# Kernel optimization log

Hardware: AMD Instinct MI355X
Metric: run time of the kernel (lower is better)

## Reference

```python
import jax, jax.numpy as jnp
import numpy as np

R = 32          # grid_res
G = 32          # num_groups
SQRT2 = 1.4142135623730951


def leaky(x):
    return jax.nn.leaky_relu(x)  # slope 0.01, same as torch default


def group_norm(x, gamma, beta, eps=1e-5):
    # x: [B, C, D, H, W]
    B, C = x.shape[0], x.shape[1]
    xr = x.reshape(B, G, -1)
    mu = xr.mean(-1, keepdims=True)
    var = xr.var(-1, keepdims=True)
    xn = ((xr - mu) * jax.lax.rsqrt(var + eps)).reshape(x.shape)
    s = (1, C, 1, 1, 1)
    return xn * gamma.reshape(s) + beta.reshape(s)


def conv3d(x, w, b):
    # x: [B,C,D,H,W], w: [O,I,k,k,k]
    y = jax.lax.conv_general_dilated(x, w, (1, 1, 1), 'SAME',
                                     dimension_numbers=('NCDHW', 'OIDHW', 'NCDHW'))
    return y + b.reshape(1, -1, 1, 1, 1)


_OFFS = jnp.array([[i, j, k] for i in (0, 1) for j in (0, 1) for k in (0, 1)], jnp.int32)  # [8,3]


def _corners(points):
    # points in [-1,1]^3 -> trilinear corner indices + weights
    coords = jnp.clip((points + 1.0) * 0.5 * (R - 1), 0.0, R - 1.0)   # [B,N,3]
    lo = jnp.clip(jnp.floor(coords), 0.0, R - 2.0)
    frac = coords - lo                                                # [B,N,3]
    lo = lo.astype(jnp.int32)
    idx3 = lo[:, :, None, :] + _OFFS[None, None]                      # [B,N,8,3]
    w = jnp.prod(jnp.where(_OFFS[None, None].astype(bool),
                           frac[:, :, None, :], 1.0 - frac[:, :, None, :]), axis=-1)  # [B,N,8]
    flat = (idx3[..., 0] * R + idx3[..., 1]) * R + idx3[..., 2]       # [B,N,8]
    return flat, w


def voxelize_points3d(points, features):
    # trilinear scatter + weight-normalized average -> [B,R,R,R,C]
    flat, w = _corners(points)
    B, _, C = features.shape

    def per_b(fl, wt, ft):
        vals = (wt[..., None] * ft[:, None, :]).reshape(-1, C)        # [N*8,C]
        g = jnp.zeros((R ** 3, C), ft.dtype).at[fl.reshape(-1)].add(vals)
        cnt = jnp.zeros((R ** 3, 1), ft.dtype).at[fl.reshape(-1)].add(wt.reshape(-1, 1))
        return g / jnp.maximum(cnt, 1e-8)

    grid = jax.vmap(per_b)(flat, w, features)                         # [B,R^3,C]
    return grid.reshape(B, R, R, R, C)


def devoxelize_points3d(points, grid):
    # trilinear gather from [B,R,R,R,C] -> [B,N,C]
    flat, w = _corners(points)
    gf = grid.reshape(grid.shape[0], R ** 3, grid.shape[-1])
    return jax.vmap(lambda fl, wt, g: jnp.einsum('nkc,nk->nc', g[fl], wt))(flat, w, gf)


def setup_inputs() -> dict:
    key = jax.random.key(0)
    ks = jax.random.split(key, 16)
    B, N, Cin, C = 8, 32768, 64, 64
    points = jax.random.uniform(ks[0], (B, N, 3), jnp.float32) * 2.0 - 1.0
    features = jax.random.normal(ks[1], (B, N, Cin), jnp.float32)
    s = 0.05
    return {
        'points': points, 'features': features,
        'w_pi': jax.random.normal(ks[2], (Cin, C), jnp.float32) * s,
        'b_pi': jnp.zeros((C,), jnp.float32),
        'w_p1': jax.random.normal(ks[3], (C, C), jnp.float32) * s,
        'b_p1': jnp.zeros((C,), jnp.float32),
        'w_p2': jax.random.normal(ks[4], (C, C), jnp.float32) * s,
        'b_p2': jnp.zeros((C,), jnp.float32),
        'g1': jnp.ones((Cin,), jnp.float32), 'be1': jnp.zeros((Cin,), jnp.float32),
        'w_c1': jax.random.normal(ks[5], (C, Cin, 3, 3, 3), jnp.float32) * s,
        'b_c1': jnp.zeros((C,), jnp.float32),
        'g2': jnp.ones((C,), jnp.float32), 'be2': jnp.zeros((C,), jnp.float32),
        'w_c2': jax.random.normal(ks[6], (C, C, 3, 3, 3), jnp.float32) * s,
        'b_c2': jnp.zeros((C,), jnp.float32),
    }


def reference(points, features, w_pi, b_pi, w_p1, b_p1, w_p2, b_p2,
              g1, be1, w_c1, b_c1, g2, be2, w_c2, b_c2):
    # voxel branch
    input_grid = jnp.moveaxis(voxelize_points3d(points, features), -1, 1)  # [B,C,R,R,R]
    g = conv3d(leaky(group_norm(input_grid, g1, be1)), w_c1, b_c1)
    g = conv3d(leaky(group_norm(g, g2, be2)), w_c2, b_c2)
    out_grid = jnp.moveaxis(g + input_grid, 1, -1) / SQRT2              # skip: input_dim == dim
    dev = devoxelize_points3d(points, out_grid)                         # [B,N,C]
    # point branch
    f0 = features @ w_pi + b_pi
    h = leaky(f0) @ w_p1 + b_p1
    h = leaky(h) @ w_p2 + b_p2
    pts = (h + f0) / SQRT2
    return (pts + dev) / SQRT2
```

## Files before the change

kernel.cpp:

```cpp
#include <hip/hip_runtime.h>


#define RSQRT2 0.70710678118654752440f

typedef float f32x4 __attribute__((ext_vector_type(4)));
typedef __bf16 bf16x8 __attribute__((ext_vector_type(8)));

static __device__ __forceinline__ unsigned short f2bf(float x) {
    union { float f; unsigned u; } v; v.f = x;
    unsigned r = v.u + 0x7FFFu + ((v.u >> 16) & 1u);
    return (unsigned short)(r >> 16);
}
static __device__ __forceinline__ float bf2f(unsigned short b) {
    union { unsigned u; float f; } v; v.u = ((unsigned)b) << 16; return v.f;
}
static __device__ __forceinline__ float leaky(float x) { return x >= 0.f ? x : 0.01f * x; }

static __device__ __forceinline__ void gload_lds16(const void* g, void* l) {
    __builtin_amdgcn_global_load_lds(
        (const __attribute__((address_space(1))) unsigned int*)g,
        (__attribute__((address_space(3))) unsigned int*)l, 16, 0, 0);
}

static __device__ __forceinline__ void corner_setup(float px, float py, float pz,
        int& lx, int& ly, int& lz, float& fx, float& fy, float& fz) {
    float cx = fminf(fmaxf((px + 1.f) * 15.5f, 0.f), 31.f);
    float cy = fminf(fmaxf((py + 1.f) * 15.5f, 0.f), 31.f);
    float cz = fminf(fmaxf((pz + 1.f) * 15.5f, 0.f), 31.f);
    lx = (int)cx; if (lx > 30) lx = 30; fx = cx - (float)lx;
    ly = (int)cy; if (ly > 30) ly = 30; fy = cy - (float)ly;
    lz = (int)cz; if (lz > 30) lz = 30; fz = cz - (float)lz;
}

__global__ __launch_bounds__(256) void wt_transform(const float* __restrict__ w,
                                                    unsigned short* __restrict__ hi,
                                                    unsigned short* __restrict__ lo) {
    int idx = blockIdx.x * 256 + threadIdx.x;
    int ko = idx >> 12;
    int co = (idx >> 6) & 63;
    int ci = idx & 63;
    float v = w[(co * 64 + ci) * 27 + ko];
    unsigned short h = f2bf(v);
    hi[idx] = h;
    lo[idx] = f2bf(v - bf2f(h));
}

__global__ __launch_bounds__(256) void mlp_wt(const float* __restrict__ w0,
                                              const float* __restrict__ w1,
                                              const float* __restrict__ w2,
                                              unsigned short* __restrict__ hi,
                                              unsigned short* __restrict__ lo) {
    int idx = blockIdx.x * 256 + threadIdx.x;
    int L = idx >> 12, rem = idx & 4095;
    int co = rem >> 6, ci = rem & 63;
    const float* s = (L == 0) ? w0 : (L == 1) ? w1 : w2;
    float v = s[ci * 64 + co];
    unsigned short h = f2bf(v);
    hi[idx] = h;
    lo[idx] = f2bf(v - bf2f(h));
}

__global__ __launch_bounds__(256) void bin_count(const float* __restrict__ pts,
                                                 int* __restrict__ cnt) {
    int p = blockIdx.x * 256 + threadIdx.x;
    int lx, ly, lz; float fx, fy, fz;
    corner_setup(pts[p * 3], pts[p * 3 + 1], pts[p * 3 + 2], lx, ly, lz, fx, fy, fz);
    int b = p >> 15;
    int rx = lx >> 2, ry = ly >> 2, rz = lz >> 2;
    int mx = (lx & 3) == 3, my = (ly & 3) == 3, mz = (lz & 3) == 3;
#pragma unroll
    for (int d = 0; d < 8; ++d) {
        int dx = d >> 2, dy = (d >> 1) & 1, dz = d & 1;
        if (dx <= mx && dy <= my && dz <= mz) {
            int bin = (b << 9) | ((rx + dx) << 6) | ((ry + dy) << 3) | (rz + dz);
            atomicAdd(&cnt[bin], 1);
        }
    }
}

__global__ __launch_bounds__(256) void bin_scan(const int* __restrict__ cnt,
                                                int* __restrict__ start,
                                                int* __restrict__ cursor) {
    __shared__ int part[256];
    int t = threadIdx.x;
    int local[16];
    int s = 0;
#pragma unroll
    for (int i = 0; i < 16; ++i) { local[i] = s; s += cnt[t * 16 + i]; }
    part[t] = s;
    __syncthreads();
    for (int off = 1; off < 256; off <<= 1) {
        int v = (t >= off) ? part[t - off] : 0;
        __syncthreads();
        part[t] += v;
        __syncthreads();
    }
    int base = (t == 0) ? 0 : part[t - 1];
#pragma unroll
    for (int i = 0; i < 16; ++i) {
        int v = base + local[i];
        start[t * 16 + i] = v;
        cursor[t * 16 + i] = v;
    }
    if (t == 255) start[4096] = part[255];
}

__global__ __launch_bounds__(256) void bin_fill(const float* __restrict__ pts,
                                                int* __restrict__ cursor,
                                                unsigned int* __restrict__ idxb,
                                                float4* __restrict__ f3) {
    int p = blockIdx.x * 256 + threadIdx.x;
    int lx, ly, lz; float fx, fy, fz;
    corner_setup(pts[p * 3], pts[p * 3 + 1], pts[p * 3 + 2], lx, ly, lz, fx, fy, fz);
    int b = p >> 15;
    int rx = lx >> 2, ry = ly >> 2, rz = lz >> 2;
    int mx = (lx & 3) == 3, my = (ly & 3) == 3, mz = (lz & 3) == 3;
    float4 fr; fr.x = fx; fr.y = fy; fr.z = fz; fr.w = 0.f;
#pragma unroll
    for (int d = 0; d < 8; ++d) {
        int dx = d >> 2, dy = (d >> 1) & 1, dz = d & 1;
        if (dx <= mx && dy <= my && dz <= mz) {
            int bin = (b << 9) | ((rx + dx) << 6) | ((ry + dy) << 3) | (rz + dz);
            int slot = atomicAdd(&cursor[bin], 1);
            unsigned ux = (unsigned)((lx & 3) - 4 * dx + 1);
            unsigned uy = (unsigned)((ly & 3) - 4 * dy + 1);
            unsigned uz = (unsigned)((lz & 3) - 4 * dz + 1);
            idxb[slot] = (unsigned)p | (ux << 18) | (uy << 21) | (uz << 24);
            f3[slot] = fr;
        }
    }
}

__global__ __launch_bounds__(256) void vox_accum(const float* __restrict__ feat,
                                                 const int* __restrict__ start,
                                                 const unsigned int* __restrict__ idxb,
                                                 const float4* __restrict__ f3,
                                                 float* __restrict__ vox,
                                                 float* __restrict__ chsum) {
    __shared__ float slab[4096];
    __shared__ float cws4[4][64];
    __shared__ float cwsum[64];
    __shared__ float rs[256], rq[256];
    int tid = threadIdx.x, lane = tid & 63, wv = tid >> 6;
    int gid = blockIdx.x;
    int b = gid >> 9, r3 = gid & 511;
    int rx = r3 >> 6, ry = (r3 >> 3) & 7, rz = r3 & 7;
    int cx0 = rx << 2, cy0 = ry << 2, cz0 = rz << 2;
    int cx = lane >> 4, cy = (lane >> 2) & 3, cz = lane & 3;

    f32x4 acc[16] = {};
    float cwr = 0.f;

    int s0 = start[gid], s1 = start[gid + 1];
    for (int e = s0 + wv; e < s1; e += 4) {
        unsigned pk = idxb[e];
        float4 fr = f3[e];
        int pid = __builtin_amdgcn_readfirstlane((int)(pk & 0x3FFFFu));
        int qx = (int)((pk >> 18) & 7u) - 1;
        int qy = (int)((pk >> 21) & 7u) - 1;
        int qz = (int)((pk >> 24) & 7u) - 1;
        float wx = (cx == qx) ? (1.f - fr.x) : ((cx == qx + 1) ? fr.x : 0.f);
        float wy = (cy == qy) ? (1.f - fr.y) : ((cy == qy + 1) ? fr.y : 0.f);
        float wz = (cz == qz) ? (1.f - fr.z) : ((cz == qz + 1) ? fr.z : 0.f);
        float w = wx * wy * wz;
        cwr += w;
        const f32x4* fp = (const f32x4*)(feat + ((size_t)pid << 6));
        f32x4 fa[8];
#pragma unroll
        for (int k = 0; k < 8; ++k) fa[k] = fp[k];
#pragma unroll
        for (int k = 0; k < 8; ++k) acc[k] += fa[k] * w;
#pragma unroll
        for (int k = 0; k < 8; ++k) fa[k] = fp[8 + k];
#pragma unroll
        for (int k = 0; k < 8; ++k) acc[8 + k] += fa[k] * w;
    }

    cws4[wv][lane] = cwr;
#pragma unroll
    for (int ph = 0; ph < 4; ++ph) {
        if (wv == ph) {
#pragma unroll
            for (int k = 0; k < 64; ++k) {
                int addr = (lane << 6) + ((k + lane) & 63);
                float v = acc[k >> 2][k & 3];
                if (ph) v += slab[addr];
                slab[addr] = v;
            }
        }
        __syncthreads();
    }
    if (tid < 64)
        cwsum[tid] = cws4[0][tid] + cws4[1][tid] + cws4[2][tid] + cws4[3][tid];
    __syncthreads();

    float s = 0.f, q = 0.f;
    for (int c = wv; c < 64; c += 4) {
        float v = slab[(c << 6) + ((lane + c) & 63)] / fmaxf(cwsum[c], 1e-8f);
        int cxx = cx0 + (c >> 4), cyy = cy0 + ((c >> 2) & 3), czz = cz0 + (c & 3);
        size_t flat = ((size_t)(b << 15)) + (size_t)((cxx << 10) | (cyy << 5) | czz);
        vox[(flat << 6) + lane] = v;
        s += v; q += v * v;
    }
    rs[tid] = s; rq[tid] = q;
    __syncthreads();
    if (tid < 64) {
        s = rs[tid] + rs[tid + 64] + rs[tid + 128] + rs[tid + 192];
        q = rq[tid] + rq[tid + 64] + rq[tid + 128] + rq[tid + 192];
        atomicAdd(&chsum[((b << 6) + tid) * 2], s);
        atomicAdd(&chsum[((b << 6) + tid) * 2 + 1], q);
    }
}

__global__ __launch_bounds__(256) void norm_stats(const float* __restrict__ src,
                                                  float* __restrict__ chsum) {
    __shared__ float rs[256], rq[256];
    int b = blockIdx.y;
    int tid = threadIdx.x;
    int c = tid & 63, rsub = tid >> 6;
    size_t rowb = ((size_t)b << 15) + (size_t)blockIdx.x * 256;
    float s = 0.f, q = 0.f;
    for (int i = 0; i < 64; ++i) {
        size_t idx = ((rowb + rsub + i * 4) << 6) + c;
        float v = src[idx];
        s += v; q += v * v;
    }
    rs[tid] = s; rq[tid] = q;
    __syncthreads();
    if (tid < 64) {
        s = rs[tid] + rs[tid + 64] + rs[tid + 128] + rs[tid + 192];
        q = rq[tid] + rq[tid + 64] + rq[tid + 128] + rq[tid + 192];
        atomicAdd(&chsum[((b << 6) + tid) * 2], s);
        atomicAdd(&chsum[((b << 6) + tid) * 2 + 1], q);
    }
}

__global__ void gn_finalize(const float* __restrict__ chsum, float* __restrict__ musr) {
    int t = threadIdx.x;
    int b = t >> 5, g = t & 31;
    float s = chsum[((b << 6) + 2 * g) * 2] + chsum[((b << 6) + 2 * g + 1) * 2];
    float q = chsum[((b << 6) + 2 * g) * 2 + 1] + chsum[((b << 6) + 2 * g + 1) * 2 + 1];
    float mu = s * (1.f / 65536.f);
    float var = q * (1.f / 65536.f) - mu * mu;
    musr[t * 2] = mu;
    musr[t * 2 + 1] = rsqrtf(var + 1e-5f);
}

__global__ __launch_bounds__(256) void gn_apply(const float* __restrict__ src,
                                                const float* __restrict__ musr,
                                                const float* __restrict__ gamma,
                                                const float* __restrict__ beta,
                                                unsigned short* __restrict__ hi,
                                                unsigned short* __restrict__ lo) {
    int i4 = blockIdx.x * 256 + threadIdx.x;
    int row = i4 >> 4;
    int b = row >> 15;
    int c0 = (i4 & 15) << 2;
    const float4 x = *(const float4*)(src + ((size_t)i4 << 2));
    float xs[4] = {x.x, x.y, x.z, x.w};
    unsigned short hs[4], ls[4];
#pragma unroll
    for (int j = 0; j < 4; ++j) {
        int c = c0 + j;
        int g = c >> 1;
        float mu = musr[((b << 5) + g) * 2];
        float rstd = musr[((b << 5) + g) * 2 + 1];
        float y = (xs[j] - mu) * rstd * gamma[c] + beta[c];
        y = leaky(y);
        hs[j] = f2bf(y);
        ls[j] = f2bf(y - bf2f(hs[j]));
    }
    ushort4 H; H.x = hs[0]; H.y = hs[1]; H.z = hs[2]; H.w = hs[3];
    ushort4 L; L.x = ls[0]; L.y = ls[1]; L.z = ls[2]; L.w = ls[3];
    *(ushort4*)(hi + ((size_t)i4 << 2)) = H;
    *(ushort4*)(lo + ((size_t)i4 << 2)) = L;
}

__global__ __launch_bounds__(256, 2) void conv3d_k(
        const unsigned short* __restrict__ Ah, const unsigned short* __restrict__ Al,
        const unsigned short* __restrict__ Wh, const unsigned short* __restrict__ Wl,
        const float* __restrict__ bias, const float* __restrict__ skip,
        float* __restrict__ out, const char* __restrict__ zp) {
    __shared__ __align__(16) unsigned short sAh[16384], sAl[16384], sWh[4096], sWl[4096];
    int tid = threadIdx.x;
    int lane = tid & 63, wave = tid >> 6;
    int wg = blockIdx.x;
    int sw = (wg & 7) * 128 + (wg >> 3);
    int b = sw >> 7, t = sw & 127;
    int w0 = (t & 3) << 3, h0 = ((t >> 2) & 3) << 3, d0 = (t >> 4) << 2;

    f32x4 acc[4][4] = {};
    const char* AhB = (const char*)Ah;
    const char* AlB = (const char*)Al;
    const char* WhB = (const char*)Wh;
    const char* WlB = (const char*)Wl;

    for (int ko = 0; ko < 27; ++ko) {
        int di = ko / 9, rem = ko - di * 9, dj = rem / 3, dk = rem - dj * 3;
        __syncthreads();
#pragma unroll
        for (int i = 0; i < 8; ++i) {
            int X = (i * 256 + tid) << 4;
            int row = X >> 7;
            int gran = ((X >> 4) & 7) ^ (row & 7);
            int d = row >> 6, h = (row >> 3) & 7, w = row & 7;
            int gd = d0 + d + di - 1, gh = h0 + h + dj - 1, gw = w0 + w + dk - 1;
            bool ok = ((unsigned)gd < 32u) & ((unsigned)gh < 32u) & ((unsigned)gw < 32u);
            size_t goff = ((((size_t)(b << 15)) +
                            (size_t)((gd << 10) + (gh << 5) + gw)) << 7) + (gran << 4);
            const char* gph = ok ? (AhB + goff) : (zp + (gran << 4));
            const char* gpl = ok ? (AlB + goff) : (zp + (gran << 4));
            int ldsoff = (i * 256 + (wave << 6)) << 4;
            gload_lds16(gph, (char*)sAh + ldsoff);
            gload_lds16(gpl, (char*)sAl + ldsoff);
        }
#pragma unroll
        for (int i = 0; i < 2; ++i) {
            int X = (i * 256 + tid) << 4;
            int row = X >> 7;
            int gran = ((X >> 4) & 7) ^ (row & 7);
            size_t goff = ((size_t)((ko << 12) + (row << 6) + (gran << 3))) << 1;
            int ldsoff = (i * 256 + (wave << 6)) << 4;
            gload_lds16(WhB + goff, (char*)sWh + ldsoff);
            gload_lds16(WlB + goff, (char*)sWl + ldsoff);
        }
        __syncthreads();
#pragma unroll
        for (int kh = 0; kh < 2; ++kh) {
            bf16x8 a_h[4], a_l[4], b_h[4], b_l[4];
#pragma unroll
            for (int mf = 0; mf < 4; ++mf) {
                int arow = (wave << 6) + (mf << 4) + (lane & 15);
                int byteoff = (arow << 7) | ((((kh << 2) | (lane >> 4)) ^ (arow & 7)) << 4);
                a_h[mf] = *(const bf16x8*)((const char*)sAh + byteoff);
                a_l[mf] = *(const bf16x8*)((const char*)sAl + byteoff);
            }
#pragma unroll
            for (int nf = 0; nf < 4; ++nf) {
                int brow = (nf << 4) + (lane & 15);
                int byteoff = (brow << 7) | ((((kh << 2) | (lane >> 4)) ^ (brow & 7)) << 4);
                b_h[nf] = *(const bf16x8*)((const char*)sWh + byteoff);
                b_l[nf] = *(const bf16x8*)((const char*)sWl + byteoff);
            }
#pragma unroll
            for (int mf = 0; mf < 4; ++mf)
#pragma unroll
                for (int nf = 0; nf < 4; ++nf) {
                    acc[mf][nf] = __builtin_amdgcn_mfma_f32_16x16x32_bf16(a_h[mf], b_h[nf], acc[mf][nf], 0, 0, 0);
                    acc[mf][nf] = __builtin_amdgcn_mfma_f32_16x16x32_bf16(a_h[mf], b_l[nf], acc[mf][nf], 0, 0, 0);
                    acc[mf][nf] = __builtin_amdgcn_mfma_f32_16x16x32_bf16(a_l[mf], b_h[nf], acc[mf][nf], 0, 0, 0);
                }
        }
    }
#pragma unroll
    for (int mf = 0; mf < 4; ++mf) {
#pragma unroll
        for (int nf = 0; nf < 4; ++nf) {
            int co = (nf << 4) + (lane & 15);
            float bv = bias[co];
#pragma unroll
            for (int r = 0; r < 4; ++r) {
                int vrow = (wave << 6) + (mf << 4) + ((lane >> 4) << 2) + r;
                int d = vrow >> 6, h = (vrow >> 3) & 7, w = vrow & 7;
                size_t flat = ((size_t)(b << 15)) +
                              (size_t)(((d0 + d) << 10) + ((h0 + h) << 5) + (w0 + w));
                size_t oi = (flat << 6) + co;
                float v = acc[mf][nf][r] + bv;
                if (skip) v = (v + skip[oi]) * RSQRT2;
                out[oi] = v;
            }
        }
    }
}

__global__ __launch_bounds__(256, 2) void point_mlp(
        const float* __restrict__ feat,
        const unsigned short* __restrict__ Mh, const unsigned short* __restrict__ Ml,
        const float* __restrict__ b0, const float* __restrict__ b1,
        const float* __restrict__ b2, float* __restrict__ pout) {
    __shared__ __align__(16) unsigned short sAh[16384], sAl[16384], sWh[4096], sWl[4096];
    int tid = threadIdx.x, lane = tid & 63, wave = tid >> 6;
    size_t pbase = (size_t)blockIdx.x << 8;

    const float4* f4 = (const float4*)(feat + (pbase << 6));
#pragma unroll
    for (int j = 0; j < 16; ++j) {
        int fidx = j * 256 + tid;
        float4 v = f4[fidx];
        float vv[4] = {v.x, v.y, v.z, v.w};
        unsigned short hh[4], ll[4];
#pragma unroll
        for (int k = 0; k < 4; ++k) { hh[k] = f2bf(vv[k]); ll[k] = f2bf(vv[k] - bf2f(hh[k])); }
        ushort4 H; H.x = hh[0]; H.y = hh[1]; H.z = hh[2]; H.w = hh[3];
        ushort4 Lo; Lo.x = ll[0]; Lo.y = ll[1]; Lo.z = ll[2]; Lo.w = ll[3];
        int Xb = fidx << 3;
        int row = Xb >> 7;
        int dest = (row << 7) | ((((Xb >> 4) & 7) ^ (row & 7)) << 4) | (Xb & 8);
        *(ushort4*)((char*)sAh + dest) = H;
        *(ushort4*)((char*)sAl + dest) = Lo;
    }

    f32x4 f0[4][4];
#pragma unroll
    for (int L = 0; L < 3; ++L) {
        __syncthreads();
#pragma unroll
        for (int i = 0; i < 2; ++i) {
            int X = (i * 256 + tid) << 4;
            int row = X >> 7;
            int gran = ((X >> 4) & 7) ^ (row & 7);
            size_t goff = ((size_t)((L << 12) + (row << 6) + (gran << 3))) << 1;
            int ldsoff = (i * 256 + (wave << 6)) << 4;
            gload_lds16((const char*)Mh + goff, (char*)sWh + ldsoff);
            gload_lds16((const char*)Ml + goff, (char*)sWl + ldsoff);
        }
        __syncthreads();
        f32x4 acc[4][4] = {};
#pragma unroll
        for (int kh = 0; kh < 2; ++kh) {
            bf16x8 a_h[4], a_l[4], b_h[4], b_l[4];
#pragma unroll
            for (int mf = 0; mf < 4; ++mf) {
                int arow = (wave << 6) + (mf << 4) + (lane & 15);
                int byteoff = (arow << 7) | ((((kh << 2) | (lane >> 4)) ^ (arow & 7)) << 4);
                a_h[mf] = *(const bf16x8*)((const char*)sAh + byteoff);
                a_l[mf] = *(const bf16x8*)((const char*)sAl + byteoff);
            }
#pragma unroll
            for (int nf = 0; nf < 4; ++nf) {
                int brow = (nf << 4) + (lane & 15);
                int byteoff = (brow << 7) | ((((kh << 2) | (lane >> 4)) ^ (brow & 7)) << 4);
                b_h[nf] = *(const bf16x8*)((const char*)sWh + byteoff);
                b_l[nf] = *(const bf16x8*)((const char*)sWl + byteoff);
            }
#pragma unroll
            for (int mf = 0; mf < 4; ++mf)
#pragma unroll
                for (int nf = 0; nf < 4; ++nf) {
                    acc[mf][nf] = __builtin_amdgcn_mfma_f32_16x16x32_bf16(a_h[mf], b_h[nf], acc[mf][nf], 0, 0, 0);
                    acc[mf][nf] = __builtin_amdgcn_mfma_f32_16x16x32_bf16(a_h[mf], b_l[nf], acc[mf][nf], 0, 0, 0);
                    acc[mf][nf] = __builtin_amdgcn_mfma_f32_16x16x32_bf16(a_l[mf], b_h[nf], acc[mf][nf], 0, 0, 0);
                }
        }
        const float* bp = (L == 0) ? b0 : (L == 1) ? b1 : b2;
        if (L < 2) {
            __syncthreads();
#pragma unroll
            for (int nf = 0; nf < 4; ++nf) {
                int col = (nf << 4) + (lane & 15);
                float bv = bp[col];
#pragma unroll
                for (int mf = 0; mf < 4; ++mf)
#pragma unroll
                    for (int r = 0; r < 4; ++r) {
                        float v = acc[mf][nf][r] + bv;
                        if (L == 0) f0[mf][nf][r] = v;
                        float a = leaky(v);
                        unsigned short h = f2bf(a);
                        unsigned short l = f2bf(a - bf2f(h));
                        int row = (wave << 6) + (mf << 4) + ((lane >> 4) << 2) + r;
                        int dest = (row << 7) | (((col >> 3) ^ (row & 7)) << 4) | ((col << 1) & 15);
                        *(unsigned short*)((char*)sAh + dest) = h;
                        *(unsigned short*)((char*)sAl + dest) = l;
                    }
            }
        } else {
#pragma unroll
            for (int nf = 0; nf < 4; ++nf) {
                int col = (nf << 4) + (lane & 15);
                float bv = bp[col];
#pragma unroll
                for (int mf = 0; mf < 4; ++mf)
#pragma unroll
                    for (int r = 0; r < 4; ++r) {
                        int row = (wave << 6) + (mf << 4) + ((lane >> 4) << 2) + r;
                        float v = (acc[mf][nf][r] + bv + f0[mf][nf][r]) * RSQRT2;
                        pout[((pbase + row) << 6) + col] = v;
                    }
            }
        }
    }
}

__global__ __launch_bounds__(256, 8) void devox_combine(
        const float* __restrict__ pts, const float* __restrict__ pmlp,
        const float* __restrict__ grid, float* __restrict__ out) {
    __shared__ int   sFl[64][8];
    __shared__ float sWt[64][8];
    int tid = threadIdx.x;
    size_t pbase = (size_t)blockIdx.x << 6;
    int b = (int)(pbase >> 15);
    if (tid < 64) {
        const float* P = pts + (pbase + tid) * 3;
        int lx, ly, lz; float fx, fy, fz;
        corner_setup(P[0], P[1], P[2], lx, ly, lz, fx, fy, fz);
        int base3 = (lx << 10) + (ly << 5) + lz;
#pragma unroll
        for (int cr = 0; cr < 8; ++cr) {
            sFl[tid][cr] = base3 + (cr >> 2) * 1024 + ((cr >> 1) & 1) * 32 + (cr & 1);
            sWt[tid][cr] = ((cr & 4) ? fx : 1.f - fx) * ((cr & 2) ? fy : 1.f - fy)
                         * ((cr & 1) ? fz : 1.f - fz);
        }
    }
    __syncthreads();
    int c = tid & 63, wv = tid >> 6;
    const float* gb = grid + (((size_t)b) << 21);
#pragma unroll 4
    for (int i = 0; i < 16; ++i) {
        int p = (wv << 4) + i;
        float dev = 0.f;
#pragma unroll
        for (int cr = 0; cr < 8; ++cr)
            dev += sWt[p][cr] * gb[(((size_t)sFl[p][cr]) << 6) + c];
        size_t oi = ((pbase + p) << 6) + c;
        out[oi] = (pmlp[oi] + dev) * RSQRT2;
    }
}

constexpr size_t OFF_VOX  = 0;
constexpr size_t OFF_GBUF = 67108864;
constexpr size_t OFF_AHI  = OFF_GBUF + 67108864;
constexpr size_t OFF_ALO  = OFF_AHI + 33554432;
constexpr size_t OFF_W1H  = OFF_ALO + 33554432;
constexpr size_t OFF_W1L  = OFF_W1H + 262144;
constexpr size_t OFF_W2H  = OFF_W1L + 262144;
constexpr size_t OFF_W2L  = OFF_W2H + 262144;
constexpr size_t OFF_CS1  = OFF_W2L + 262144;
constexpr size_t OFF_CS2  = OFF_CS1 + 4096;
constexpr size_t OFF_MS1  = OFF_CS2 + 4096;
constexpr size_t OFF_MS2  = OFF_MS1 + 2048;
constexpr size_t OFF_BCNT = OFF_MS2 + 2048;
constexpr size_t OFF_BSTA = OFF_BCNT + 16384;
constexpr size_t OFF_BCUR = OFF_BSTA + 20480;
constexpr size_t OFF_IDX  = OFF_BCUR + 16384;
constexpr size_t OFF_ZP   = OFF_IDX + 8388608;
constexpr size_t OFF_MWH  = OFF_ZP + 256;
constexpr size_t OFF_MWL  = OFF_MWH + 24576;
constexpr size_t OFF_END  = OFF_MWL + 24576;

extern "C" void kernel_launch(void* const* d_in, const int* in_sizes, int n_in,
                              void* d_out, int out_size, void* d_ws, size_t ws_size,
                              hipStream_t stream) {
    const float* points = (const float*)d_in[0];
    const float* feat   = (const float*)d_in[1];
    const float* w_pi = (const float*)d_in[2];
    const float* b_pi = (const float*)d_in[3];
    const float* w_p1 = (const float*)d_in[4];
    const float* b_p1 = (const float*)d_in[5];
    const float* w_p2 = (const float*)d_in[6];
    const float* b_p2 = (const float*)d_in[7];
    const float* g1   = (const float*)d_in[8];
    const float* be1  = (const float*)d_in[9];
    const float* w_c1 = (const float*)d_in[10];
    const float* b_c1 = (const float*)d_in[11];
    const float* g2   = (const float*)d_in[12];
    const float* be2  = (const float*)d_in[13];
    const float* w_c2 = (const float*)d_in[14];
    const float* b_c2 = (const float*)d_in[15];

    char* ws = (char*)d_ws;
    float* vox  = (float*)(ws + OFF_VOX);
    float* gbuf = (float*)(ws + OFF_GBUF);
    unsigned short* ahi = (unsigned short*)(ws + OFF_AHI);
    unsigned short* alo = (unsigned short*)(ws + OFF_ALO);
    float4* f3  = (float4*)(ws + OFF_AHI);
    float* pmlp = (float*)(ws + OFF_AHI);
    unsigned short* w1h = (unsigned short*)(ws + OFF_W1H);
    unsigned short* w1l = (unsigned short*)(ws + OFF_W1L);
    unsigned short* w2h = (unsigned short*)(ws + OFF_W2H);
    unsigned short* w2l = (unsigned short*)(ws + OFF_W2L);
    float* cs1 = (float*)(ws + OFF_CS1);
    float* cs2 = (float*)(ws + OFF_CS2);
    float* ms1 = (float*)(ws + OFF_MS1);
    float* ms2 = (float*)(ws + OFF_MS2);
    int* bcnt = (int*)(ws + OFF_BCNT);
    int* bsta = (int*)(ws + OFF_BSTA);
    int* bcur = (int*)(ws + OFF_BCUR);
    unsigned int* idxb = (unsigned int*)(ws + OFF_IDX);
    char* zp  = ws + OFF_ZP;
    unsigned short* mwh = (unsigned short*)(ws + OFF_MWH);
    unsigned short* mwl = (unsigned short*)(ws + OFF_MWL);

    hipMemsetAsync(ws + OFF_CS1, 0, 12288, stream);
    hipMemsetAsync(ws + OFF_BCNT, 0, 16384, stream);
    hipMemsetAsync(ws + OFF_ZP, 0, 256, stream);

    wt_transform<<<432, 256, 0, stream>>>(w_c1, w1h, w1l);
    wt_transform<<<432, 256, 0, stream>>>(w_c2, w2h, w2l);
    mlp_wt<<<48, 256, 0, stream>>>(w_pi, w_p1, w_p2, mwh, mwl);

    bin_count<<<1024, 256, 0, stream>>>(points, bcnt);
    bin_scan<<<1, 256, 0, stream>>>(bcnt, bsta, bcur);
    bin_fill<<<1024, 256, 0, stream>>>(points, bcur, idxb, f3);
    vox_accum<<<4096, 256, 0, stream>>>(feat, bsta, idxb, f3, vox, cs1);

    gn_finalize<<<1, 256, 0, stream>>>(cs1, ms1);
    gn_apply<<<16384, 256, 0, stream>>>(vox, ms1, g1, be1, ahi, alo);
    conv3d_k<<<1024, 256, 0, stream>>>(ahi, alo, w1h, w1l, b_c1, nullptr, gbuf, zp);

    norm_stats<<<dim3(128, 8), 256, 0, stream>>>(gbuf, cs2);
    gn_finalize<<<1, 256, 0, stream>>>(cs2, ms2);
    gn_apply<<<16384, 256, 0, stream>>>(gbuf, ms2, g2, be2, ahi, alo);
    conv3d_k<<<1024, 256, 0, stream>>>(ahi, alo, w2h, w2l, b_c2, vox, gbuf, zp);

    point_mlp<<<1024, 256, 0, stream>>>(feat, mwh, mwl, b_pi, b_p1, b_p2, pmlp);
    devox_combine<<<4096, 256, 0, stream>>>(points, pmlp, gbuf, (float*)d_out);
}
```

Measured before the change: 948.6 us.

## Compute voxel scatter accumulation with split-bf16 MFMA matrix products

Replaces the per-entry scalar FMA accumulation in vox_accum with chunks of 64 entries. Each chunk stages features and trilinear weights into LDS as hi/lo bf16 pairs and is reduced with three bf16 MFMA products per tile, approximating fp32 precision. The goal is to move the channel-by-cell weighted sum onto matrix cores and to drop the serialized four-phase LDS reduction across waves. In exchange it adds bf16 split conversions, extra LDS traffic, two barriers per chunk, and wasted work from padding partial chunks.

Result: no change. 933.8 us (-1.6%).

```diff
diff --git a/kernel.cpp b/kernel.cpp
--- a/kernel.cpp
+++ b/kernel.cpp
@@ -5,6 +5,7 @@
 
 typedef float f32x4 __attribute__((ext_vector_type(4)));
 typedef __bf16 bf16x8 __attribute__((ext_vector_type(8)));
+typedef unsigned short u16x8 __attribute__((ext_vector_type(8)));
 
 static __device__ __forceinline__ unsigned short f2bf(float x) {
     union { float f; unsigned u; } v; v.f = x;
@@ -137,6 +138,7 @@
                                                  const float4* __restrict__ f3,
                                                  float* __restrict__ vox,
                                                  float* __restrict__ chsum) {
+    __shared__ __align__(16) unsigned short Fh[4096], Fl[4096], Wh[4096], Wl[4096];
     __shared__ float slab[4096];
     __shared__ float cws4[4][64];
     __shared__ float cwsum[64];
@@ -148,48 +150,85 @@
     int cx0 = rx << 2, cy0 = ry << 2, cz0 = rz << 2;
     int cx = lane >> 4, cy = (lane >> 2) & 3, cz = lane & 3;
 
-    f32x4 acc[16] = {};
+    f32x4 acc[4] = {};
     float cwr = 0.f;
 
     int s0 = start[gid], s1 = start[gid + 1];
-    for (int e = s0 + wv; e < s1; e += 4) {
-        unsigned pk = idxb[e];
-        float4 fr = f3[e];
-        int pid = __builtin_amdgcn_readfirstlane((int)(pk & 0x3FFFFu));
-        int qx = (int)((pk >> 18) & 7u) - 1;
-        int qy = (int)((pk >> 21) & 7u) - 1;
-        int qz = (int)((pk >> 24) & 7u) - 1;
-        float wx = (cx == qx) ? (1.f - fr.x) : ((cx == qx + 1) ? fr.x : 0.f);
-        float wy = (cy == qy) ? (1.f - fr.y) : ((cy == qy + 1) ? fr.y : 0.f);
-        float wz = (cz == qz) ? (1.f - fr.z) : ((cz == qz + 1) ? fr.z : 0.f);
-        float w = wx * wy * wz;
-        cwr += w;
-        const f32x4* fp = (const f32x4*)(feat + ((size_t)pid << 6));
-        f32x4 fa[8];
-#pragma unroll
-        for (int k = 0; k < 8; ++k) fa[k] = fp[k];
-#pragma unroll
-        for (int k = 0; k < 8; ++k) acc[k] += fa[k] * w;
-#pragma unroll
-        for (int k = 0; k < 8; ++k) fa[k] = fp[8 + k];
-#pragma unroll
-        for (int k = 0; k < 8; ++k) acc[8 + k] += fa[k] * w;
+    int nch = (s1 - s0 + 63) >> 6;
+    for (int c = 0; c < nch; ++c) {
+        float vals[16], wgt[16];
+        int ebase = s0 + (c << 6) + (wv << 4);
+#pragma unroll
+        for (int j = 0; j < 16; ++j) {
+            int eg = ebase + j;
+            int ee = (eg < s1) ? eg : s0;
+            unsigned pk = idxb[ee];
+            float4 fr = f3[ee];
+            int pid = (int)(pk & 0x3FFFFu);
+            vals[j] = feat[((size_t)pid << 6) + lane];
+            int qx = (int)((pk >> 18) & 7u) - 1;
+            int qy = (int)((pk >> 21) & 7u) - 1;
+            int qz = (int)((pk >> 24) & 7u) - 1;
+            float wx = (cx == qx) ? (1.f - fr.x) : ((cx == qx + 1) ? fr.x : 0.f);
+            float wy = (cy == qy) ? (1.f - fr.y) : ((cy == qy + 1) ? fr.y : 0.f);
+            float wz = (cz == qz) ? (1.f - fr.z) : ((cz == qz + 1) ? fr.z : 0.f);
+            float w = wx * wy * wz;
+            if (eg >= s1) w = 0.f;
+            wgt[j] = w;
+            cwr += w;
+        }
+#pragma unroll
+        for (int g = 0; g < 2; ++g) {
+            u16x8 FH, FL, WH, WL;
+#pragma unroll
+            for (int j = 0; j < 8; ++j) {
+                float v = vals[g * 8 + j];
+                unsigned short h = f2bf(v);
+                FH[j] = h; FL[j] = f2bf(v - bf2f(h));
+                float w = wgt[g * 8 + j];
+                unsigned short h2 = f2bf(w);
+                WH[j] = h2; WL[j] = f2bf(w - bf2f(h2));
+            }
+            int gran = (wv << 1) | g;
+            int dst = (lane << 7) | ((gran ^ (lane & 7)) << 4);
+            *(u16x8*)((char*)Fh + dst) = FH;
+            *(u16x8*)((char*)Fl + dst) = FL;
+            *(u16x8*)((char*)Wh + dst) = WH;
+            *(u16x8*)((char*)Wl + dst) = WL;
+        }
+        __syncthreads();
+#pragma unroll
+        for (int kh = 0; kh < 2; ++kh) {
+            int ks = (kh << 2) | (lane >> 4);
+            int arow = (wv << 4) + (lane & 15);
+            int aoff = (arow << 7) | ((ks ^ (arow & 7)) << 4);
+            bf16x8 ah = *(const bf16x8*)((const char*)Fh + aoff);
+            bf16x8 al = *(const bf16x8*)((const char*)Fl + aoff);
+#pragma unroll
+            for (int nf = 0; nf < 4; ++nf) {
+                int brow = (nf << 4) + (lane & 15);
+                int boff = (brow << 7) | ((ks ^ (brow & 7)) << 4);
+                bf16x8 bh = *(const bf16x8*)((const char*)Wh + boff);
+                bf16x8 bl = *(const bf16x8*)((const char*)Wl + boff);
+                acc[nf] = __builtin_amdgcn_mfma_f32_16x16x32_bf16(ah, bh, acc[nf], 0, 0, 0);
+                acc[nf] = __builtin_amdgcn_mfma_f32_16x16x32_bf16(ah, bl, acc[nf], 0, 0, 0);
+                acc[nf] = __builtin_amdgcn_mfma_f32_16x16x32_bf16(al, bh, acc[nf], 0, 0, 0);
+            }
+        }
+        __syncthreads();
     }
 
     cws4[wv][lane] = cwr;
 #pragma unroll
-    for (int ph = 0; ph < 4; ++ph) {
-        if (wv == ph) {
-#pragma unroll
-            for (int k = 0; k < 64; ++k) {
-                int addr = (lane << 6) + ((k + lane) & 63);
-                float v = acc[k >> 2][k & 3];
-                if (ph) v += slab[addr];
-                slab[addr] = v;
-            }
-        }
-        __syncthreads();
-    }
+    for (int nf = 0; nf < 4; ++nf) {
+        int cell = (nf << 4) + (lane & 15);
+#pragma unroll
+        for (int r = 0; r < 4; ++r) {
+            int ch = (wv << 4) + ((lane >> 4) << 2) + r;
+            slab[(cell << 6) + ((ch + cell) & 63)] = acc[nf][r];
+        }
+    }
+    __syncthreads();
     if (tid < 64)
         cwsum[tid] = cws4[0][tid] + cws4[1][tid] + cws4[2][tid] + cws4[3][tid];
     __syncthreads();
```
